# Optimization experiments

Hardware: AMD Instinct MI355X
Metric: run time of the kernel (lower is better)

Reference implementation:

```python
import jax, jax.numpy as jnp
import numpy as np

B, Q, K, QS, KS, H, DV = 16, 128, 512, 256, 256, 128, 256


def setup_inputs() -> dict:
    key = jax.random.key(0)
    ks = jax.random.split(key, 7)
    return {
        "queries": jax.random.normal(ks[0], (B, Q, QS), dtype=jnp.float32),
        "keys": jax.random.normal(ks[1], (B, K, KS), dtype=jnp.float32),
        "values": jax.random.normal(ks[2], (B, K, DV), dtype=jnp.float32),
        "valid_lens": jax.random.randint(ks[3], (B,), 1, K + 1),
        # Linear weights (no bias); stored as [in, hidden] so x @ W == nn.Linear
        "W_q": jax.random.normal(ks[4], (QS, H), dtype=jnp.float32) / np.float32(np.sqrt(QS)),
        "W_k": jax.random.normal(ks[5], (KS, H), dtype=jnp.float32) / np.float32(np.sqrt(KS)),
        "w_v": jax.random.normal(ks[6], (H,), dtype=jnp.float32) / np.float32(np.sqrt(H)),
    }


def reference(queries, keys, values, valid_lens, W_q, W_k, w_v):
    # Projections
    q = jnp.einsum('bqd,dh->bqh', queries, W_q)   # [B,Q,H]
    k = jnp.einsum('bkd,dh->bkh', keys, W_k)      # [B,K,H]
    # Additive (Bahdanau) score: tanh(q + k) . w_v  -> [B,Q,K]
    feats = jnp.tanh(q[:, :, None, :] + k[:, None, :, :])  # [B,Q,K,H] big intermediate
    scores = jnp.einsum('bqkh,h->bqk', feats, w_v)
    # masked softmax over keys: positions >= valid_len get -1e6 (as in torch ref)
    mask = jnp.arange(K)[None, None, :] < valid_lens[:, None, None]  # [B,1,K] bcast
    scores = jnp.where(mask, scores, jnp.float32(-1e6))
    attn = jax.nn.softmax(scores, axis=-1)        # [B,Q,K]
    # dropout p=0.0 -> identity
    return jnp.einsum('bqk,bkd->bqd', attn, values)  # [B,Q,DV]
```

## Files before the change

kernel.cpp:

```cpp
#include <hip/hip_runtime.h>
#include <hip/hip_bf16.h>

#define NB 16
#define NQ 128
#define NK 512
#define DIN 256
#define NH 128
#define NDV 256

#define CSC 2.8853900817779268f

__global__ __launch_bounds__(256) void proj_both_kernel(
    const float* __restrict__ Q, const float* __restrict__ K,
    const float* __restrict__ Wq, const float* __restrict__ Wk,
    const int* __restrict__ vlen,
    float* __restrict__ EQ, float* __restrict__ EKT)
{
    __shared__ float Xl[32 * DIN];
    __shared__ float Wl[64 * NH];
    const int tid = threadIdx.x;
    int blk = blockIdx.x;
    const float* X; const float* W;
    int b, r0, isq;
    if (blk < 64) { isq = 1; b = blk & 15; r0 = (blk >> 4) * 32;
                    X = Q + ((size_t)b * NQ + r0) * DIN; W = Wq; }
    else { blk -= 64; isq = 0; b = blk & 15; r0 = (blk >> 4) * 32;
           X = K + ((size_t)b * NK + r0) * DIN; W = Wk;
           int vl = vlen[b]; vl = vl < 1 ? 1 : (vl > NK ? NK : vl);
           if (r0 >= vl) return;
    }

    {
        const float4* Xg = (const float4*)X;
        float4* Xs = (float4*)Xl;
        #pragma unroll
        for (int i = 0; i < 8; ++i) Xs[tid + 256 * i] = Xg[tid + 256 * i];
    }

    const int h4 = tid & 31;
    const int rg = tid >> 5;
    const float4* Wg = (const float4*)W;
    float4* Ws4 = (float4*)Wl;

    float4 acc[4];
    #pragma unroll
    for (int r = 0; r < 4; ++r) { acc[r].x = 0.f; acc[r].y = 0.f; acc[r].z = 0.f; acc[r].w = 0.f; }

    float4 pre[8];
    #pragma unroll
    for (int j = 0; j < 8; ++j) pre[j] = Wg[tid + 256 * j];
    #pragma unroll
    for (int j = 0; j < 8; ++j) Ws4[tid + 256 * j] = pre[j];

    for (int c = 0; c < 4; ++c) {
        if (c < 3) {
            #pragma unroll
            for (int j = 0; j < 8; ++j) pre[j] = Wg[(c + 1) * 2048 + tid + 256 * j];
        }
        __syncthreads();

        const float* Xc = &Xl[c * 64];
        #pragma unroll 4
        for (int dd = 0; dd < 64; dd += 4) {
            float4 w0 = *(const float4*)&Wl[(dd + 0) * NH + 4 * h4];
            float4 w1 = *(const float4*)&Wl[(dd + 1) * NH + 4 * h4];
            float4 w2 = *(const float4*)&Wl[(dd + 2) * NH + 4 * h4];
            float4 w3 = *(const float4*)&Wl[(dd + 3) * NH + 4 * h4];
            #pragma unroll
            for (int r = 0; r < 4; ++r) {
                float4 x = *(const float4*)&Xc[(rg * 4 + r) * DIN + dd];
                acc[r].x += x.x * w0.x + x.y * w1.x + x.z * w2.x + x.w * w3.x;
                acc[r].y += x.x * w0.y + x.y * w1.y + x.z * w2.y + x.w * w3.y;
                acc[r].z += x.x * w0.z + x.y * w1.z + x.z * w2.z + x.w * w3.z;
                acc[r].w += x.x * w0.w + x.y * w1.w + x.z * w2.w + x.w * w3.w;
            }
        }
        __syncthreads();
        if (c < 3) {
            #pragma unroll
            for (int j = 0; j < 8; ++j) Ws4[tid + 256 * j] = pre[j];
        }
    }

    #pragma unroll
    for (int r = 0; r < 4; ++r) {
        acc[r].x = __builtin_amdgcn_exp2f(CSC * acc[r].x);
        acc[r].y = __builtin_amdgcn_exp2f(CSC * acc[r].y);
        acc[r].z = __builtin_amdgcn_exp2f(CSC * acc[r].z);
        acc[r].w = __builtin_amdgcn_exp2f(CSC * acc[r].w);
    }

    if (isq) {
        #pragma unroll
        for (int r = 0; r < 4; ++r)
            *(float4*)&EQ[((size_t)b * NQ + r0 + rg * 4 + r) * NH + 4 * h4] = acc[r];
    } else {
        float* T = Xl;
        __syncthreads();
        #pragma unroll
        for (int r = 0; r < 4; ++r) {
            T[(4 * h4 + 0) * 36 + rg * 4 + r] = acc[r].x;
            T[(4 * h4 + 1) * 36 + rg * 4 + r] = acc[r].y;
            T[(4 * h4 + 2) * 36 + rg * 4 + r] = acc[r].z;
            T[(4 * h4 + 3) * 36 + rg * 4 + r] = acc[r].w;
        }
        __syncthreads();
        #pragma unroll
        for (int i = 0; i < 4; ++i) {
            const int idx = tid + 256 * i;
            const int h = idx >> 3, c8 = idx & 7;
            float4 v = *(const float4*)&T[h * 36 + c8 * 4];
            *(float4*)&EKT[((size_t)b * NH + h) * NK + r0 + c8 * 4] = v;
        }
    }
}

__global__ __launch_bounds__(512, 2) void attn_fused_kernel(
    const float* __restrict__ EQ, const float* __restrict__ EKT,
    const float* __restrict__ wv, const int* __restrict__ vlen,
    const float* __restrict__ V, float* __restrict__ OUT)
{
    __shared__ float eq4[NH * 4];
    __shared__ float wvl[NH];
    __shared__ float sc4[NK * 4];
    __shared__ float part[4][4][NDV];
    const int tid = threadIdx.x;
    const int b  = blockIdx.x & 15;
    const int q0 = (blockIdx.x >> 4) * 4;

    {
        const int r = tid >> 7, h = tid & 127;
        eq4[h * 4 + r] = EQ[((size_t)b * NQ + q0 + r) * NH + h];
    }
    if (tid < NH) wvl[tid] = -2.0f * wv[tid];
    __syncthreads();

    int vl = vlen[b];
    vl = vl < 1 ? 1 : (vl > NK ? NK : vl);

    {
        float a0 = 0.f, a1 = 0.f, a2 = 0.f, a3 = 0.f;
        const bool vld = (tid < vl);
        if (vld) {
            const float* kb = EKT + (size_t)b * NH * NK + tid;
            #pragma unroll 8
            for (int h = 0; h < NH; h += 2) {
                float ek0 = kb[(size_t)h * NK];
                float ek1 = kb[(size_t)(h + 1) * NK];
                float4 ea = *(const float4*)&eq4[h * 4];
                float4 eb = *(const float4*)&eq4[(h + 1) * 4];
                float w0 = wvl[h], w1 = wvl[h + 1];
                {
                    float y0 = __builtin_fmaf(ea.x, ek0, 1.0f);
                    float y1 = __builtin_fmaf(eb.x, ek1, 1.0f);
                    float n  = __builtin_fmaf(w0, y1, w1 * y0);
                    a0 = __builtin_fmaf(n, __builtin_amdgcn_rcpf(y0 * y1), a0);
                }
                {
                    float y0 = __builtin_fmaf(ea.y, ek0, 1.0f);
                    float y1 = __builtin_fmaf(eb.y, ek1, 1.0f);
                    float n  = __builtin_fmaf(w0, y1, w1 * y0);
                    a1 = __builtin_fmaf(n, __builtin_amdgcn_rcpf(y0 * y1), a1);
                }
                {
                    float y0 = __builtin_fmaf(ea.z, ek0, 1.0f);
                    float y1 = __builtin_fmaf(eb.z, ek1, 1.0f);
                    float n  = __builtin_fmaf(w0, y1, w1 * y0);
                    a2 = __builtin_fmaf(n, __builtin_amdgcn_rcpf(y0 * y1), a2);
                }
                {
                    float y0 = __builtin_fmaf(ea.w, ek0, 1.0f);
                    float y1 = __builtin_fmaf(eb.w, ek1, 1.0f);
                    float n  = __builtin_fmaf(w0, y1, w1 * y0);
                    a3 = __builtin_fmaf(n, __builtin_amdgcn_rcpf(y0 * y1), a3);
                }
            }
        }
        float4 sv;
        sv.x = vld ? a0 : -1e6f;
        sv.y = vld ? a1 : -1e6f;
        sv.z = vld ? a2 : -1e6f;
        sv.w = vld ? a3 : -1e6f;
        *(float4*)&sc4[tid * 4] = sv;
    }
    __syncthreads();

    const int w = tid >> 6, lane = tid & 63;
    if (w < 4) {
        float vals[8];
        float m = -3.0e38f;
        #pragma unroll
        for (int i = 0; i < 8; ++i) { vals[i] = sc4[(lane + 64 * i) * 4 + w]; m = fmaxf(m, vals[i]); }
        #pragma unroll
        for (int off = 32; off; off >>= 1) m = fmaxf(m, __shfl_xor(m, off, 64));
        float s = 0.f;
        #pragma unroll
        for (int i = 0; i < 8; ++i) {
            vals[i] = __builtin_amdgcn_exp2f((vals[i] - m) * 1.4426950408889634f);
            s += vals[i];
        }
        #pragma unroll
        for (int off = 32; off; off >>= 1) s += __shfl_xor(s, off, 64);
        const float invs = 1.0f / s;
        #pragma unroll
        for (int i = 0; i < 8; ++i) sc4[(lane + 64 * i) * 4 + w] = vals[i] * invs;
    }
    __syncthreads();

    float4 o[4];
    #pragma unroll
    for (int r = 0; r < 4; ++r) { o[r].x = 0.f; o[r].y = 0.f; o[r].z = 0.f; o[r].w = 0.f; }
    {
        const int kb0 = w * 64;
        if (kb0 < vl) {
            const int kn = (vl - kb0 < 64) ? (vl - kb0) : 64;
            const float* vb = V + (size_t)b * NK * NDV + lane * 4;
            #pragma unroll 8
            for (int kk = 0; kk < kn; ++kk) {
                const int k = kb0 + kk;
                float4 v4 = *(const float4*)(vb + (size_t)k * NDV);
                float4 p  = *(const float4*)&sc4[k * 4];
                o[0].x += p.x * v4.x; o[0].y += p.x * v4.y; o[0].z += p.x * v4.z; o[0].w += p.x * v4.w;
                o[1].x += p.y * v4.x; o[1].y += p.y * v4.y; o[1].z += p.y * v4.z; o[1].w += p.y * v4.w;
                o[2].x += p.z * v4.x; o[2].y += p.z * v4.y; o[2].z += p.z * v4.z; o[2].w += p.z * v4.w;
                o[3].x += p.w * v4.x; o[3].y += p.w * v4.y; o[3].z += p.w * v4.z; o[3].w += p.w * v4.w;
            }
        }
    }
    if (w >= 4) {
        #pragma unroll
        for (int r = 0; r < 4; ++r) *(float4*)&part[w - 4][r][lane * 4] = o[r];
    }
    __syncthreads();
    if (w < 4) {
        #pragma unroll
        for (int r = 0; r < 4; ++r) {
            float4 t = *(const float4*)&part[w][r][lane * 4];
            o[r].x += t.x; o[r].y += t.y; o[r].z += t.z; o[r].w += t.w;
            *(float4*)&part[w][r][lane * 4] = o[r];
        }
    }
    __syncthreads();
    if (tid < 256) {
        const int r = tid >> 6, d4 = tid & 63;
        float4 s = {0.f, 0.f, 0.f, 0.f};
        #pragma unroll
        for (int p = 0; p < 4; ++p) {
            float4 q = *(const float4*)&part[p][r][d4 * 4];
            s.x += q.x; s.y += q.y; s.z += q.z; s.w += q.w;
        }
        *(float4*)&OUT[((size_t)b * NQ + q0 + r) * NDV + d4 * 4] = s;
    }
}

extern "C" void kernel_launch(void* const* d_in, const int* in_sizes, int n_in,
                              void* d_out, int out_size, void* d_ws, size_t ws_size,
                              hipStream_t stream) {
    const float* queries = (const float*)d_in[0];
    const float* keys    = (const float*)d_in[1];
    const float* values  = (const float*)d_in[2];
    const int*   vlen    = (const int*)d_in[3];
    const float* Wq      = (const float*)d_in[4];
    const float* Wk      = (const float*)d_in[5];
    const float* wv      = (const float*)d_in[6];
    float* out           = (float*)d_out;

    float* eq  = (float*)d_ws;
    float* ekt = eq + (size_t)NB * NQ * NH;

    proj_both_kernel<<<64 + 256, 256, 0, stream>>>(queries, keys, Wq, Wk, vlen, eq, ekt);
    attn_fused_kernel<<<NB * 32, 512, 0, stream>>>(eq, ekt, wv, vlen, values, out);
}
```

Before: 121.0 us.

## Halve projection row tile and split reduction dimension across thread halves

The projection kernel now processes 16 rows per block instead of 32, which doubles the grid to 640 blocks. To keep all 256 threads busy, the input dimension is split in two, with each half of the block accumulating over its own 128-wide slice. The two partial sums are then combined through shared memory before the exp and the store. This raises block count and parallelism and lowers shared memory per block, which should help occupancy on the 256 CUs. The cost is an extra reduction step and synchronization, plus each block reloading the full weight matrix, which doubles total weight traffic.

Result: no change. 122.0 us (+0.8%).

```diff
diff --git a/kernel.cpp b/kernel.cpp
--- a/kernel.cpp
+++ b/kernel.cpp
@@ -16,15 +16,15 @@
     const int* __restrict__ vlen,
     float* __restrict__ EQ, float* __restrict__ EKT)
 {
-    __shared__ float Xl[32 * DIN];
-    __shared__ float Wl[64 * NH];
+    __shared__ float Xl[16 * DIN];
+    __shared__ float Wl[2 * 32 * NH];
     const int tid = threadIdx.x;
     int blk = blockIdx.x;
     const float* X; const float* W;
     int b, r0, isq;
-    if (blk < 64) { isq = 1; b = blk & 15; r0 = (blk >> 4) * 32;
-                    X = Q + ((size_t)b * NQ + r0) * DIN; W = Wq; }
-    else { blk -= 64; isq = 0; b = blk & 15; r0 = (blk >> 4) * 32;
+    if (blk < 128) { isq = 1; b = blk & 15; r0 = (blk >> 4) * 16;
+                     X = Q + ((size_t)b * NQ + r0) * DIN; W = Wq; }
+    else { blk -= 128; isq = 0; b = blk & 15; r0 = (blk >> 4) * 16;
            X = K + ((size_t)b * NK + r0) * DIN; W = Wk;
            int vl = vlen[b]; vl = vl < 1 ? 1 : (vl > NK ? NK : vl);
            if (r0 >= vl) return;
@@ -34,11 +34,13 @@
         const float4* Xg = (const float4*)X;
         float4* Xs = (float4*)Xl;
         #pragma unroll
-        for (int i = 0; i < 8; ++i) Xs[tid + 256 * i] = Xg[tid + 256 * i];
-    }
-
-    const int h4 = tid & 31;
-    const int rg = tid >> 5;
+        for (int i = 0; i < 4; ++i) Xs[tid + 256 * i] = Xg[tid + 256 * i];
+    }
+
+    const int h4  = tid & 31;
+    const int rg  = tid >> 5;
+    const int dh  = rg >> 2;
+    const int rgl = rg & 3;
     const float4* Wg = (const float4*)W;
     float4* Ws4 = (float4*)Wl;
 
@@ -48,27 +50,34 @@
 
     float4 pre[8];
     #pragma unroll
-    for (int j = 0; j < 8; ++j) pre[j] = Wg[tid + 256 * j];
-    #pragma unroll
-    for (int j = 0; j < 8; ++j) Ws4[tid + 256 * j] = pre[j];
-
-    for (int c = 0; c < 4; ++c) {
-        if (c < 3) {
-            #pragma unroll
-            for (int j = 0; j < 8; ++j) pre[j] = Wg[(c + 1) * 2048 + tid + 256 * j];
+    for (int j = 0; j < 4; ++j) pre[j]     = Wg[tid + 256 * j];
+    #pragma unroll
+    for (int j = 0; j < 4; ++j) pre[4 + j] = Wg[4096 + tid + 256 * j];
+    #pragma unroll
+    for (int j = 0; j < 4; ++j) Ws4[tid + 256 * j]        = pre[j];
+    #pragma unroll
+    for (int j = 0; j < 4; ++j) Ws4[1024 + tid + 256 * j] = pre[4 + j];
+
+    for (int s = 0; s < 4; ++s) {
+        if (s < 3) {
+            #pragma unroll
+            for (int j = 0; j < 4; ++j) pre[j]     = Wg[1024 * (s + 1) + tid + 256 * j];
+            #pragma unroll
+            for (int j = 0; j < 4; ++j) pre[4 + j] = Wg[4096 + 1024 * (s + 1) + tid + 256 * j];
         }
         __syncthreads();
 
-        const float* Xc = &Xl[c * 64];
+        const float* Wc = &Wl[dh * 4096];
+        const float* Xc = &Xl[dh * 128 + s * 32];
         #pragma unroll 4
-        for (int dd = 0; dd < 64; dd += 4) {
-            float4 w0 = *(const float4*)&Wl[(dd + 0) * NH + 4 * h4];
-            float4 w1 = *(const float4*)&Wl[(dd + 1) * NH + 4 * h4];
-            float4 w2 = *(const float4*)&Wl[(dd + 2) * NH + 4 * h4];
-            float4 w3 = *(const float4*)&Wl[(dd + 3) * NH + 4 * h4];
+        for (int dd = 0; dd < 32; dd += 4) {
+            float4 w0 = *(const float4*)&Wc[(dd + 0) * NH + 4 * h4];
+            float4 w1 = *(const float4*)&Wc[(dd + 1) * NH + 4 * h4];
+            float4 w2 = *(const float4*)&Wc[(dd + 2) * NH + 4 * h4];
+            float4 w3 = *(const float4*)&Wc[(dd + 3) * NH + 4 * h4];
             #pragma unroll
             for (int r = 0; r < 4; ++r) {
-                float4 x = *(const float4*)&Xc[(rg * 4 + r) * DIN + dd];
+                float4 x = *(const float4*)&Xc[(rgl * 4 + r) * DIN + dd];
                 acc[r].x += x.x * w0.x + x.y * w1.x + x.z * w2.x + x.w * w3.x;
                 acc[r].y += x.x * w0.y + x.y * w1.y + x.z * w2.y + x.w * w3.y;
                 acc[r].z += x.x * w0.z + x.y * w1.z + x.z * w2.z + x.w * w3.z;
@@ -76,41 +85,55 @@
             }
         }
         __syncthreads();
-        if (c < 3) {
-            #pragma unroll
-            for (int j = 0; j < 8; ++j) Ws4[tid + 256 * j] = pre[j];
-        }
-    }
-
-    #pragma unroll
-    for (int r = 0; r < 4; ++r) {
-        acc[r].x = __builtin_amdgcn_exp2f(CSC * acc[r].x);
-        acc[r].y = __builtin_amdgcn_exp2f(CSC * acc[r].y);
-        acc[r].z = __builtin_amdgcn_exp2f(CSC * acc[r].z);
-        acc[r].w = __builtin_amdgcn_exp2f(CSC * acc[r].w);
+        if (s < 3) {
+            #pragma unroll
+            for (int j = 0; j < 4; ++j) Ws4[tid + 256 * j]        = pre[j];
+            #pragma unroll
+            for (int j = 0; j < 4; ++j) Ws4[1024 + tid + 256 * j] = pre[4 + j];
+        }
+    }
+
+    float* Red = Xl;
+    if (dh == 1) {
+        #pragma unroll
+        for (int r = 0; r < 4; ++r) *(float4*)&Red[(tid - 128) * 16 + r * 4] = acc[r];
+    }
+    __syncthreads();
+    if (dh == 0) {
+        #pragma unroll
+        for (int r = 0; r < 4; ++r) {
+            float4 t = *(const float4*)&Red[tid * 16 + r * 4];
+            acc[r].x = __builtin_amdgcn_exp2f(CSC * (acc[r].x + t.x));
+            acc[r].y = __builtin_amdgcn_exp2f(CSC * (acc[r].y + t.y));
+            acc[r].z = __builtin_amdgcn_exp2f(CSC * (acc[r].z + t.z));
+            acc[r].w = __builtin_amdgcn_exp2f(CSC * (acc[r].w + t.w));
+        }
     }
 
     if (isq) {
-        #pragma unroll
-        for (int r = 0; r < 4; ++r)
-            *(float4*)&EQ[((size_t)b * NQ + r0 + rg * 4 + r) * NH + 4 * h4] = acc[r];
+        if (dh == 0) {
+            #pragma unroll
+            for (int r = 0; r < 4; ++r)
+                *(float4*)&EQ[((size_t)b * NQ + r0 + rgl * 4 + r) * NH + 4 * h4] = acc[r];
+        }
     } else {
-        float* T = Xl;
+        float* T = Wl;
+        if (dh == 0) {
+            #pragma unroll
+            for (int r = 0; r < 4; ++r) {
+                T[(4 * h4 + 0) * 20 + rgl * 4 + r] = acc[r].x;
+                T[(4 * h4 + 1) * 20 + rgl * 4 + r] = acc[r].y;
+                T[(4 * h4 + 2) * 20 + rgl * 4 + r] = acc[r].z;
+                T[(4 * h4 + 3) * 20 + rgl * 4 + r] = acc[r].w;
+            }
+        }
         __syncthreads();
         #pragma unroll
-        for (int r = 0; r < 4; ++r) {
-            T[(4 * h4 + 0) * 36 + rg * 4 + r] = acc[r].x;
-            T[(4 * h4 + 1) * 36 + rg * 4 + r] = acc[r].y;
-            T[(4 * h4 + 2) * 36 + rg * 4 + r] = acc[r].z;
-            T[(4 * h4 + 3) * 36 + rg * 4 + r] = acc[r].w;
-        }
-        __syncthreads();
-        #pragma unroll
-        for (int i = 0; i < 4; ++i) {
+        for (int i = 0; i < 2; ++i) {
             const int idx = tid + 256 * i;
-            const int h = idx >> 3, c8 = idx & 7;
-            float4 v = *(const float4*)&T[h * 36 + c8 * 4];
-            *(float4*)&EKT[((size_t)b * NH + h) * NK + r0 + c8 * 4] = v;
+            const int h = idx >> 2, c4 = idx & 3;
+            float4 v = *(const float4*)&T[h * 20 + c4 * 4];
+            *(float4*)&EKT[((size_t)b * NH + h) * NK + r0 + c4 * 4] = v;
         }
     }
 }
@@ -268,6 +291,6 @@
     float* eq  = (float*)d_ws;
     float* ekt = eq + (size_t)NB * NQ * NH;
 
-    proj_both_kernel<<<64 + 256, 256, 0, stream>>>(queries, keys, Wq, Wk, vlen, eq, ekt);
+    proj_both_kernel<<<128 + 512, 256, 0, stream>>>(queries, keys, Wq, Wk, vlen, eq, ekt);
     attn_fused_kernel<<<NB * 32, 512, 0, stream>>>(eq, ekt, wv, vlen, values, out);
 }
```
